# Kernel optimization log

Hardware: AMD Instinct MI355X
Metric: run time of the kernel (lower is better)

The kernel has to match this reference:

```python
import jax, jax.numpy as jnp
import numpy as np

EPS = 1e-12


def setup_inputs() -> dict:
    key = jax.random.key(0)
    k1, k2, k3 = jax.random.split(key, 3)
    N, D, K = 262144, 64, 1024
    input_data = jax.random.normal(k1, (N, D), dtype=jnp.float32)
    random_vector = jax.random.normal(k2, (N, D), dtype=jnp.float32)
    # HeUniform over (K, D): limit = sqrt(6 / fan_in) with fan_in = K
    limit = np.sqrt(6.0 / K)
    codebooks = jax.random.uniform(k3, (K, D), dtype=jnp.float32, minval=-limit, maxval=limit)
    codebooks_used = jnp.zeros((K,), dtype=jnp.int32)
    return {"input_data": input_data, "random_vector": random_vector,
            "codebooks": codebooks, "codebooks_used": codebooks_used}


def reference(input_data, random_vector, codebooks, codebooks_used):
    # training=True path of NSVQ.call
    K = codebooks.shape[0]
    N = input_data.shape[0]
    sim = input_data @ codebooks.T
    dists = (jnp.sum(input_data * input_data, axis=1, keepdims=True)
             + jnp.sum(codebooks * codebooks, axis=1)[None, :]
             - 2.0 * sim)
    min_indices = jnp.argmin(dists, axis=1)                      # [N]
    hard_q = codebooks[min_indices]                              # [N, D]
    # NSVQ noise substitution
    res_norm = jnp.sqrt(jnp.sum((input_data - hard_q) ** 2, axis=1, keepdims=True))
    rv_norm = jnp.sqrt(jnp.sum(random_vector ** 2, axis=1, keepdims=True))
    vq_error = (res_norm / (rv_norm + EPS)) * random_vector
    quantized_input = input_data + vq_error
    # perplexity from code usage histogram
    counts = jax.ops.segment_sum(jnp.ones((N,), dtype=jnp.float32), min_indices,
                                 num_segments=K)                 # [K]
    avg_probs = counts / jnp.float32(N)
    perplexity = jnp.exp(-jnp.sum(avg_probs * jnp.log(avg_probs + EPS)))
    codebooks_used_new = codebooks_used + counts.astype(jnp.int32)
    return quantized_input, perplexity, codebooks_used_new
```

## Files before the change

kernel.cpp:

```cpp
#include <hip/hip_runtime.h>
#include <math.h>


#define NROWS 262144
#define DIM 64
#define KCODES 1024
#define ND ((size_t)NROWS * DIM)

typedef __attribute__((ext_vector_type(8))) _Float16 f16x8;
typedef __attribute__((ext_vector_type(4))) float f32x4;

typedef const __attribute__((address_space(1))) void* as1p;
typedef __attribute__((address_space(3))) void* as3p;
__device__ inline void gl_lds16(const void* g, void* l) {
    __builtin_amdgcn_global_load_lds((as1p)g, (as3p)l, 16, 0, 0);
}

__global__ __launch_bounds__(256) void nsvq_prep(
    const float* __restrict__ cb, _Float16* __restrict__ cbs,
    float* __restrict__ cnorm, unsigned int* __restrict__ counts)
{
    const int tid = blockIdx.x * 256 + threadIdx.x;
    if (tid < KCODES) counts[tid] = 0u;
    const int k = tid >> 3;
    const int u = tid & 7;
    const float* p = cb + (size_t)k * DIM + u * 8;
    float4 f0 = *(const float4*)p;
    float4 f1 = *(const float4*)(p + 4);
    float fv[8] = {f0.x, f0.y, f0.z, f0.w, f1.x, f1.y, f1.z, f1.w};

    float s = 0.f;
    f16x8 hv, lv;
#pragma unroll
    for (int j = 0; j < 8; ++j) {
        s = fmaf(fv[j], fv[j], s);
        float m2 = -2.0f * fv[j];
        _Float16 h = (_Float16)m2;
        hv[j] = h;
        lv[j] = (_Float16)(m2 - (float)h);
    }
#pragma unroll
    for (int o = 1; o < 8; o <<= 1) s += __shfl_xor(s, o, 64);

    const size_t base = (size_t)(k >> 6) * 8192 + (size_t)u * 512 + (size_t)(k & 63) * 8;
    *(f16x8*)(cbs + base) = hv;
    *(f16x8*)(cbs + base + 4096) = lv;
    if (u == 0) cnorm[k] = s;
}

__global__ __launch_bounds__(512, 4) void nsvq_fused(
    const float* __restrict__ x, const float* __restrict__ rv,
    const _Float16* __restrict__ cbs, const float* __restrict__ cnorm,
    float* __restrict__ out, unsigned int* __restrict__ counts)
{
    __shared__ _Float16 lds[16384];

    const int tid  = threadIdx.x;
    const int lane = tid & 63;
    const int wave = tid >> 6;
    const int q    = lane >> 4;
    const int n    = lane & 15;
    const int wBase = blockIdx.x * 256 + wave * 32;

#pragma unroll
    for (int r = 0; r < 2; ++r) {
        const int off = (r * 512 + tid) * 8;
        gl_lds16(cbs + off, lds + off);
    }

    f16x8 ah[2][2], al[2][2];
    float xx[2];
#pragma unroll
    for (int s = 0; s < 2; ++s) {
        const int row = wBase + s * 16 + n;
        const float* px = x + (size_t)row * DIM + q * 8;
        float acc = 0.f;
#pragma unroll
        for (int c2 = 0; c2 < 2; ++c2) {
            float4 g0 = *(const float4*)(px + c2 * 32);
            float4 g1 = *(const float4*)(px + c2 * 32 + 4);
            float fv[8] = {g0.x, g0.y, g0.z, g0.w, g1.x, g1.y, g1.z, g1.w};
#pragma unroll
            for (int j = 0; j < 8; ++j) {
                float f = fv[j];
                acc = fmaf(f, f, acc);
                _Float16 h = (_Float16)f;
                ah[s][c2][j] = h;
                al[s][c2][j] = (_Float16)(f - (float)h);
            }
        }
        acc += __shfl_xor(acc, 16, 64);
        acc += __shfl_xor(acc, 32, 64);
        xx[s] = acc;
    }

    float cn_cur[4], cn_nxt[4];
#pragma unroll
    for (int t = 0; t < 4; ++t) cn_cur[t] = cnorm[t * 16 + n];

    float best[2][4];
    int   bidx[2][4];
#pragma unroll
    for (int s = 0; s < 2; ++s)
#pragma unroll
        for (int r = 0; r < 4; ++r) { best[s][r] = 3.4e38f; bidx[s][r] = 0; }

    __syncthreads();

    auto compute_chunk = [&](int b, int cbase) {
        const _Float16* buf = lds + b * 8192;
#pragma unroll
        for (int t = 0; t < 4; ++t) {
            const int ci = (t * 16 + n) * 8;
            f16x8 bh0 = *(const f16x8*)(buf + q * 512 + ci);
            f16x8 bh1 = *(const f16x8*)(buf + (q + 4) * 512 + ci);
            f16x8 bl0 = *(const f16x8*)(buf + 4096 + q * 512 + ci);
            f16x8 bl1 = *(const f16x8*)(buf + 4096 + (q + 4) * 512 + ci);
            const int code = cbase + t * 16 + n;
#pragma unroll
            for (int s = 0; s < 2; ++s) {
                f32x4 a = {cn_cur[t], cn_cur[t], cn_cur[t], cn_cur[t]};
                a = __builtin_amdgcn_mfma_f32_16x16x32_f16(ah[s][0], bh0, a, 0, 0, 0);
                a = __builtin_amdgcn_mfma_f32_16x16x32_f16(ah[s][1], bh1, a, 0, 0, 0);
                a = __builtin_amdgcn_mfma_f32_16x16x32_f16(al[s][0], bh0, a, 0, 0, 0);
                a = __builtin_amdgcn_mfma_f32_16x16x32_f16(al[s][1], bh1, a, 0, 0, 0);
                a = __builtin_amdgcn_mfma_f32_16x16x32_f16(ah[s][0], bl0, a, 0, 0, 0);
                a = __builtin_amdgcn_mfma_f32_16x16x32_f16(ah[s][1], bl1, a, 0, 0, 0);
#pragma unroll
                for (int r = 0; r < 4; ++r) {
                    if (a[r] < best[s][r]) { best[s][r] = a[r]; bidx[s][r] = code; }
                }
            }
        }
    };

    for (int c = 0; c < 15; ++c) {
        const int b = c & 1;
        {
            const _Float16* src = cbs + (size_t)(c + 1) * 8192;
            _Float16* dst = lds + (b ^ 1) * 8192;
#pragma unroll
            for (int r = 0; r < 2; ++r) {
                const int off = (r * 512 + tid) * 8;
                gl_lds16(src + off, dst + off);
            }
#pragma unroll
            for (int t = 0; t < 4; ++t) cn_nxt[t] = cnorm[(c + 1) * 64 + t * 16 + n];
        }
        compute_chunk(b, c * 64);
        __syncthreads();
#pragma unroll
        for (int t = 0; t < 4; ++t) cn_cur[t] = cn_nxt[t];
    }
    compute_chunk(1, 15 * 64);

#pragma unroll
    for (int o = 1; o < 16; o <<= 1) {
#pragma unroll
        for (int s = 0; s < 2; ++s)
#pragma unroll
            for (int r = 0; r < 4; ++r) {
                float od = __shfl_xor(best[s][r], o, 64);
                int   ok = __shfl_xor(bidx[s][r], o, 64);
                if (od < best[s][r] || (od == best[s][r] && ok < bidx[s][r])) {
                    best[s][r] = od; bidx[s][r] = ok;
                }
            }
    }
    if (n == 0) {
#pragma unroll
        for (int s = 0; s < 2; ++s)
#pragma unroll
            for (int r = 0; r < 4; ++r) atomicAdd(&counts[bidx[s][r]], 1u);
    }

    const int src = ((n >> 2) << 4) | n;
#pragma unroll
    for (int s = 0; s < 2; ++s) {
        float w0 = __shfl(best[s][0], src, 64);
        float w1 = __shfl(best[s][1], src, 64);
        float w2 = __shfl(best[s][2], src, 64);
        float w3 = __shfl(best[s][3], src, 64);
        float wa = (n & 1) ? w1 : w0;
        float wb = (n & 1) ? w3 : w2;
        float dmin = (n & 2) ? wb : wa;

        float res2 = xx[s] + dmin;
        if (res2 < 0.f) res2 = 0.f;
        const float resn = sqrtf(res2);

        const int row = wBase + s * 16 + n;
        const float* pr = rv + (size_t)row * DIM + q * 8;
        float rvf[16];
        float rr = 0.f;
#pragma unroll
        for (int c2 = 0; c2 < 2; ++c2) {
            float4 g0 = *(const float4*)(pr + c2 * 32);
            float4 g1 = *(const float4*)(pr + c2 * 32 + 4);
            rvf[c2 * 8 + 0] = g0.x; rvf[c2 * 8 + 1] = g0.y;
            rvf[c2 * 8 + 2] = g0.z; rvf[c2 * 8 + 3] = g0.w;
            rvf[c2 * 8 + 4] = g1.x; rvf[c2 * 8 + 5] = g1.y;
            rvf[c2 * 8 + 6] = g1.z; rvf[c2 * 8 + 7] = g1.w;
#pragma unroll
            for (int j = 0; j < 8; ++j) rr = fmaf(rvf[c2 * 8 + j], rvf[c2 * 8 + j], rr);
        }
        rr += __shfl_xor(rr, 16, 64);
        rr += __shfl_xor(rr, 32, 64);
        const float scale = resn / (sqrtf(rr) + 1e-12f);

        float* po = out + (size_t)row * DIM + q * 8;
#pragma unroll
        for (int c2 = 0; c2 < 2; ++c2) {
            float4 o0, o1;
            o0.x = fmaf(scale, rvf[c2 * 8 + 0], (float)ah[s][c2][0] + (float)al[s][c2][0]);
            o0.y = fmaf(scale, rvf[c2 * 8 + 1], (float)ah[s][c2][1] + (float)al[s][c2][1]);
            o0.z = fmaf(scale, rvf[c2 * 8 + 2], (float)ah[s][c2][2] + (float)al[s][c2][2]);
            o0.w = fmaf(scale, rvf[c2 * 8 + 3], (float)ah[s][c2][3] + (float)al[s][c2][3]);
            o1.x = fmaf(scale, rvf[c2 * 8 + 4], (float)ah[s][c2][4] + (float)al[s][c2][4]);
            o1.y = fmaf(scale, rvf[c2 * 8 + 5], (float)ah[s][c2][5] + (float)al[s][c2][5]);
            o1.z = fmaf(scale, rvf[c2 * 8 + 6], (float)ah[s][c2][6] + (float)al[s][c2][6]);
            o1.w = fmaf(scale, rvf[c2 * 8 + 7], (float)ah[s][c2][7] + (float)al[s][c2][7]);
            *(float4*)(po + c2 * 32) = o0;
            *(float4*)(po + c2 * 32 + 4) = o1;
        }
    }
}

__global__ void nsvq_finalize(const unsigned int* __restrict__ counts,
                              const int* __restrict__ used,
                              float* __restrict__ out)
{
    const int k = threadIdx.x;
    const unsigned c = counts[k];
    float avg = (float)c * (1.0f / (float)NROWS);
    float term = (c > 0) ? (-avg * logf(avg + 1e-12f)) : 0.0f;

    float v = term;
#pragma unroll
    for (int o = 32; o > 0; o >>= 1) v += __shfl_down(v, o, 64);

    __shared__ float partial[16];
    if ((threadIdx.x & 63) == 0) partial[threadIdx.x >> 6] = v;
    __syncthreads();

    if (threadIdx.x < 64) {
        float s = (threadIdx.x < 16) ? partial[threadIdx.x] : 0.0f;
#pragma unroll
        for (int o = 32; o > 0; o >>= 1) s += __shfl_down(s, o, 64);
        if (threadIdx.x == 0) out[ND] = expf(s);
    }
    out[ND + 1 + k] = (float)(c + (unsigned)used[k]);
}

extern "C" void kernel_launch(void* const* d_in, const int* in_sizes, int n_in,
                              void* d_out, int out_size, void* d_ws, size_t ws_size,
                              hipStream_t stream) {
    const float* x    = (const float*)d_in[0];
    const float* rv   = (const float*)d_in[1];
    const float* cb   = (const float*)d_in[2];
    const int*   used = (const int*)d_in[3];
    float* out = (float*)d_out;

    char* ws = (char*)d_ws;
    unsigned int* counts = (unsigned int*)ws;
    float*        cnorm  = (float*)(ws + 4096);
    _Float16*     cbs    = (_Float16*)(ws + 8192);

    nsvq_prep<<<KCODES * 8 / 256, 256, 0, stream>>>(cb, cbs, cnorm, counts);
    nsvq_fused<<<NROWS / 256, 512, 0, stream>>>(x, rv, cbs, cnorm, out, counts);
    nsvq_finalize<<<1, KCODES, 0, stream>>>(counts, used, out);
}
```

Measured before the change: 280.6 us.

## Drop LDS staging; single-wave blocks read codebook directly from global/L2

The fused kernel moves from 512-thread blocks that double-buffer codebook chunks in LDS with barriers to 64-thread single-wave blocks. Each block handles 64 rows (four 16-row MFMA tiles instead of two) and loads codebook fragments straight from global memory through the cache. The aim is to remove LDS staging and __syncthreads overhead and to double B-fragment reuse per load. In exchange, every wave now issues its own global loads for the whole codebook, so speed depends on L2/L1 bandwidth and latency hiding. Register pressure also rises from the doubled accumulator and A-fragment state.

```diff
diff --git a/kernel.cpp b/kernel.cpp
--- a/kernel.cpp
+++ b/kernel.cpp
@@ -9,12 +9,6 @@
 
 typedef __attribute__((ext_vector_type(8))) _Float16 f16x8;
 typedef __attribute__((ext_vector_type(4))) float f32x4;
-
-typedef const __attribute__((address_space(1))) void* as1p;
-typedef __attribute__((address_space(3))) void* as3p;
-__device__ inline void gl_lds16(const void* g, void* l) {
-    __builtin_amdgcn_global_load_lds((as1p)g, (as3p)l, 16, 0, 0);
-}
 
 __global__ __launch_bounds__(256) void nsvq_prep(
     const float* __restrict__ cb, _Float16* __restrict__ cbs,
@@ -48,30 +42,20 @@
     if (u == 0) cnorm[k] = s;
 }
 
-__global__ __launch_bounds__(512, 4) void nsvq_fused(
+__global__ __launch_bounds__(64, 3) void nsvq_fused(
     const float* __restrict__ x, const float* __restrict__ rv,
     const _Float16* __restrict__ cbs, const float* __restrict__ cnorm,
     float* __restrict__ out, unsigned int* __restrict__ counts)
 {
-    __shared__ _Float16 lds[16384];
-
-    const int tid  = threadIdx.x;
-    const int lane = tid & 63;
-    const int wave = tid >> 6;
+    const int lane = threadIdx.x;
     const int q    = lane >> 4;
     const int n    = lane & 15;
-    const int wBase = blockIdx.x * 256 + wave * 32;
-
-#pragma unroll
-    for (int r = 0; r < 2; ++r) {
-        const int off = (r * 512 + tid) * 8;
-        gl_lds16(cbs + off, lds + off);
-    }
-
-    f16x8 ah[2][2], al[2][2];
-    float xx[2];
-#pragma unroll
-    for (int s = 0; s < 2; ++s) {
+    const int wBase = blockIdx.x * 64;
+
+    f16x8 ah[4][2], al[4][2];
+    float xx[4];
+#pragma unroll
+    for (int s = 0; s < 4; ++s) {
         const int row = wBase + s * 16 + n;
         const float* px = x + (size_t)row * DIM + q * 8;
         float acc = 0.f;
@@ -94,32 +78,31 @@
         xx[s] = acc;
     }
 
-    float cn_cur[4], cn_nxt[4];
-#pragma unroll
-    for (int t = 0; t < 4; ++t) cn_cur[t] = cnorm[t * 16 + n];
-
-    float best[2][4];
-    int   bidx[2][4];
-#pragma unroll
-    for (int s = 0; s < 2; ++s)
+    float best[4][4];
+    int   bidx[4][4];
+#pragma unroll
+    for (int s = 0; s < 4; ++s)
 #pragma unroll
         for (int r = 0; r < 4; ++r) { best[s][r] = 3.4e38f; bidx[s][r] = 0; }
 
-    __syncthreads();
-
-    auto compute_chunk = [&](int b, int cbase) {
-        const _Float16* buf = lds + b * 8192;
+#pragma unroll 2
+    for (int c = 0; c < 16; ++c) {
+        const _Float16* src = cbs + (size_t)c * 8192;
+        float cn[4];
+#pragma unroll
+        for (int t = 0; t < 4; ++t) cn[t] = cnorm[c * 64 + t * 16 + n];
+
 #pragma unroll
         for (int t = 0; t < 4; ++t) {
             const int ci = (t * 16 + n) * 8;
-            f16x8 bh0 = *(const f16x8*)(buf + q * 512 + ci);
-            f16x8 bh1 = *(const f16x8*)(buf + (q + 4) * 512 + ci);
-            f16x8 bl0 = *(const f16x8*)(buf + 4096 + q * 512 + ci);
-            f16x8 bl1 = *(const f16x8*)(buf + 4096 + (q + 4) * 512 + ci);
-            const int code = cbase + t * 16 + n;
-#pragma unroll
-            for (int s = 0; s < 2; ++s) {
-                f32x4 a = {cn_cur[t], cn_cur[t], cn_cur[t], cn_cur[t]};
+            f16x8 bh0 = *(const f16x8*)(src + q * 512 + ci);
+            f16x8 bh1 = *(const f16x8*)(src + (q + 4) * 512 + ci);
+            f16x8 bl0 = *(const f16x8*)(src + 4096 + q * 512 + ci);
+            f16x8 bl1 = *(const f16x8*)(src + 4096 + (q + 4) * 512 + ci);
+            const int code = c * 64 + t * 16 + n;
+#pragma unroll
+            for (int s = 0; s < 4; ++s) {
+                f32x4 a = {cn[t], cn[t], cn[t], cn[t]};
                 a = __builtin_amdgcn_mfma_f32_16x16x32_f16(ah[s][0], bh0, a, 0, 0, 0);
                 a = __builtin_amdgcn_mfma_f32_16x16x32_f16(ah[s][1], bh1, a, 0, 0, 0);
                 a = __builtin_amdgcn_mfma_f32_16x16x32_f16(al[s][0], bh0, a, 0, 0, 0);
@@ -132,32 +115,12 @@
                 }
             }
         }
-    };
-
-    for (int c = 0; c < 15; ++c) {
-        const int b = c & 1;
-        {
-            const _Float16* src = cbs + (size_t)(c + 1) * 8192;
-            _Float16* dst = lds + (b ^ 1) * 8192;
-#pragma unroll
-            for (int r = 0; r < 2; ++r) {
-                const int off = (r * 512 + tid) * 8;
-                gl_lds16(src + off, dst + off);
-            }
-#pragma unroll
-            for (int t = 0; t < 4; ++t) cn_nxt[t] = cnorm[(c + 1) * 64 + t * 16 + n];
-        }
-        compute_chunk(b, c * 64);
-        __syncthreads();
-#pragma unroll
-        for (int t = 0; t < 4; ++t) cn_cur[t] = cn_nxt[t];
-    }
-    compute_chunk(1, 15 * 64);
+    }
 
 #pragma unroll
     for (int o = 1; o < 16; o <<= 1) {
 #pragma unroll
-        for (int s = 0; s < 2; ++s)
+        for (int s = 0; s < 4; ++s)
 #pragma unroll
             for (int r = 0; r < 4; ++r) {
                 float od = __shfl_xor(best[s][r], o, 64);
@@ -169,14 +132,14 @@
     }
     if (n == 0) {
 #pragma unroll
-        for (int s = 0; s < 2; ++s)
+        for (int s = 0; s < 4; ++s)
 #pragma unroll
             for (int r = 0; r < 4; ++r) atomicAdd(&counts[bidx[s][r]], 1u);
     }
 
     const int src = ((n >> 2) << 4) | n;
 #pragma unroll
-    for (int s = 0; s < 2; ++s) {
+    for (int s = 0; s < 4; ++s) {
         float w0 = __shfl(best[s][0], src, 64);
         float w1 = __shfl(best[s][1], src, 64);
         float w2 = __shfl(best[s][2], src, 64);
@@ -267,6 +230,6 @@
     _Float16*     cbs    = (_Float16*)(ws + 8192);
 
     nsvq_prep<<<KCODES * 8 / 256, 256, 0, stream>>>(cb, cbs, cnorm, counts);
-    nsvq_fused<<<NROWS / 256, 512, 0, stream>>>(x, rv, cbs, cnorm, out, counts);
+    nsvq_fused<<<NROWS / 64, 64, 0, stream>>>(x, rv, cbs, cnorm, out, counts);
     nsvq_finalize<<<1, KCODES, 0, stream>>>(counts, used, out);
 }
```

Result: slower. 338.3 us (+20.6%).
